# Kernel tuning notes

Hardware: AMD Instinct MI355X
Metric: run time of the kernel (lower is better)

The kernel has to match this reference:

```python
import jax, jax.numpy as jnp
import numpy as np

EMBED = 1024
HEADS = 16
HEAD_DIM = EMBED // HEADS


def setup_inputs() -> dict:
    key = jax.random.key(0)
    k1, k2, k3, k4, k5 = jax.random.split(key, 5)
    x = jax.random.normal(k1, (2, 2048, EMBED), dtype=jnp.float32)
    # torch nn.Linear params: weight [out, in], bias [out]; y = x @ W.T + b
    s_attn = 1.0 / np.sqrt(EMBED)
    w_attn = jax.random.uniform(k2, (3 * EMBED, EMBED), jnp.float32, -s_attn, s_attn)
    b_attn = jax.random.uniform(k3, (3 * EMBED,), jnp.float32, -s_attn, s_attn)
    w_proj = jax.random.uniform(k4, (EMBED, EMBED), jnp.float32, -s_attn, s_attn)
    b_proj = jax.random.uniform(k5, (EMBED,), jnp.float32, -s_attn, s_attn)
    return {"x": x, "w_attn": w_attn, "b_attn": b_attn, "w_proj": w_proj, "b_proj": b_proj}


def reference(x, w_attn, b_attn, w_proj, b_proj):
    B, S, D = x.shape
    qkv = x @ w_attn.T + b_attn                      # [B, S, 3D]
    q, k, v = jnp.split(qkv, 3, axis=-1)             # each [B, S, D]

    def heads(t):  # [B, S, D] -> [B, H, S, hd]
        return t.reshape(B, S, HEADS, HEAD_DIM).transpose(0, 2, 1, 3)

    q, k, v = heads(q), heads(k), heads(v)
    # Faithful to source: NO 1/sqrt(d) scaling, NO causal mask.
    w = jnp.einsum('bhqd,bhkd->bhqk', q, k)          # [B, H, S, S]
    w = jax.nn.softmax(w, axis=-1)
    a = jnp.einsum('bhqk,bhkd->bhqd', w, v)          # [B, H, S, hd]
    a = a.transpose(0, 2, 1, 3).reshape(B, S, D)     # merge heads
    return a @ w_proj.T + b_proj
```

## Files before the change

kernel.cpp:

```cpp
#include <hip/hip_runtime.h>
#include <hip/hip_bf16.h>
#include <stdint.h>
#include <math.h>


typedef __attribute__((ext_vector_type(2))) float f32x2;
typedef __attribute__((ext_vector_type(4))) float f32x4;
typedef __attribute__((ext_vector_type(16))) float f32x16;
typedef __attribute__((ext_vector_type(8))) short bf16x8;

static __device__ __forceinline__ unsigned short f2bf(float f) {
    unsigned u = __float_as_uint(f);
    u += 0x7FFFu + ((u >> 16) & 1u);
    return (unsigned short)(u >> 16);
}
static __device__ __forceinline__ unsigned cvt_pk_bf16(float a, float b) {
    unsigned r;
    asm("v_cvt_pk_bf16_f32 %0, %1, %2" : "=v"(r) : "v"(a), "v"(b));
    return r;
}
static __device__ __forceinline__ float fexp2(float x) {
    float r;
    asm("v_exp_f32 %0, %1" : "=v"(r) : "v"(x));
    return r;
}

typedef const __attribute__((address_space(1))) unsigned int* gas_ptr;
typedef __attribute__((address_space(3))) unsigned int* las_ptr;
static __device__ __forceinline__ void gload_lds16(const void* g, void* l) {
    __builtin_amdgcn_global_load_lds((gas_ptr)g, (las_ptr)l, 16, 0, 0);
}

__global__ void conv_all_kernel(const float* __restrict__ x,
                                const float* __restrict__ wa,
                                unsigned short* __restrict__ x1,
                                unsigned short* __restrict__ w1a) {
    int i = blockIdx.x * blockDim.x + threadIdx.x;
    int stride = gridDim.x * blockDim.x;
    for (; i < 1835008; i += stride) {
        const float* s; unsigned short* d; int j;
        if (i < 1048576)      { s = x;  d = x1;  j = i; }
        else                  { s = wa; d = w1a; j = i - 1048576; }
        float4 v = ((const float4*)s)[j];
        ushort4 o;
        o.x = f2bf(v.x); o.y = f2bf(v.y); o.z = f2bf(v.z); o.w = f2bf(v.w);
        ((ushort4*)d)[j] = o;
    }
}

__global__ __launch_bounds__(256, 2) void gemm_qkv_kernel(
    const unsigned short* __restrict__ A,
    const unsigned short* __restrict__ Bw,
    const float* __restrict__ bias,
    unsigned short* __restrict__ q1,
    unsigned short* __restrict__ k1,
    unsigned short* __restrict__ vT,
    int N, int K)
{
    __shared__ __align__(16) unsigned char lds[34816];
    const int t  = threadIdx.x;
    const int lane = t & 63;
    const int w  = t >> 6;
    const int wr = w >> 1, wc = w & 1;
    const int lg = lane >> 4, ll = lane & 15;

    const int gx = gridDim.x;
    const int flat = blockIdx.y * gx + blockIdx.x;
    const int cpx = (gx * gridDim.y) >> 3;
    const int swz = (flat & 7) * cpx + (flat >> 3);
    const int m0 = (swz / gx) * 128;
    const int n0 = (swz % gx) * 128;

    f32x4 acc[4][4] = {};

    const int srow  = t >> 3;
    const int sslot = t & 7;
    const unsigned short* Abase[4];
    const unsigned short* Bbase[4];
#pragma unroll
    for (int ci = 0; ci < 4; ++ci) {
        int r  = ci * 32 + srow;
        int cg = sslot ^ (r & 7);
        Abase[ci] = A  + (size_t)(m0 + r) * K + cg * 8;
        Bbase[ci] = Bw + (size_t)(n0 + r) * K + cg * 8;
    }

    for (int k0 = 0; k0 < K; k0 += 64) {
#pragma unroll
        for (int ci = 0; ci < 4; ++ci)
            gload_lds16(Abase[ci] + k0, lds + ci*4096 + (t>>6)*1024);
#pragma unroll
        for (int ci = 0; ci < 4; ++ci)
            gload_lds16(Bbase[ci] + k0, lds + 16384 + ci*4096 + (t>>6)*1024);
        __syncthreads();

        bf16x8 af[4][2], bfr[4][2];
#pragma unroll
        for (int mt = 0; mt < 4; ++mt)
#pragma unroll
            for (int kc = 0; kc < 2; ++kc) {
                int row = wr*64 + mt*16 + ll;
                int cg  = (4*kc + lg) ^ (row & 7);
                af[mt][kc] = *(const bf16x8*)(lds + row*128 + cg*16);
            }
#pragma unroll
        for (int nt = 0; nt < 4; ++nt)
#pragma unroll
            for (int kc = 0; kc < 2; ++kc) {
                int row = wc*64 + nt*16 + ll;
                int cg  = (4*kc + lg) ^ (row & 7);
                bfr[nt][kc] = *(const bf16x8*)(lds + 16384 + row*128 + cg*16);
            }
#pragma unroll
        for (int kc = 0; kc < 2; ++kc)
#pragma unroll
            for (int mt = 0; mt < 4; ++mt)
#pragma unroll
                for (int nt = 0; nt < 4; ++nt)
                    acc[mt][nt] = __builtin_amdgcn_mfma_f32_16x16x32_bf16(
                        af[mt][kc], bfr[nt][kc], acc[mt][nt], 0, 0, 0);
        __syncthreads();
    }

    const int TYPE = n0 >> 10;
    unsigned short* l16 = (unsigned short*)lds;
#pragma unroll
    for (int mt = 0; mt < 4; ++mt)
#pragma unroll
      for (int nt = 0; nt < 4; ++nt)
#pragma unroll
        for (int r = 0; r < 4; ++r) {
            int mp = wr*64 + mt*16 + 4*lg + r;
            int np = wc*64 + nt*16 + ll;
            float v = acc[mt][nt][r] + bias[n0 + np];
            if (TYPE == 0) v *= 1.44269504f;
            unsigned short h16 = f2bf(v);
            if (TYPE == 2) l16[np*136 + mp] = h16;
            else           l16[mp*136 + np] = h16;
        }
    __syncthreads();
    {
        const int r2 = t >> 1, half = t & 1;
        const unsigned short* src = l16 + r2*136 + half*64;
        unsigned short* dst;
        if (TYPE == 2) {
            int n = n0 + r2;
            int h = (n >> 6) & 15, d = n & 63;
            int bb = m0 >> 11;
            dst = vT + ((size_t)(bb*16 + h)*64 + d)*2048 + (m0 & 2047) + half*64;
        } else {
            int m = m0 + r2;
            int bb = m >> 11, s = m & 2047;
            int h = ((n0 + half*64) >> 6) & 15;
            dst = (TYPE == 0 ? q1 : k1) + ((size_t)(bb*16 + h)*2048 + s)*64;
        }
#pragma unroll
        for (int j = 0; j < 8; ++j)
            *(uint4*)(dst + j*8) = *(const uint4*)(src + j*8);
    }
}

__global__ __launch_bounds__(256, 2) void gemm_proj_kernel(
    const unsigned short* __restrict__ A,
    const unsigned short* __restrict__ Bw,
    const float* __restrict__ bias,
    float* __restrict__ outp)
{
    __shared__ __align__(16) unsigned char lds[24576];
    const int t  = threadIdx.x;
    const int lane = t & 63;
    const int w  = t >> 6;
    const int lg = lane >> 4, ll = lane & 15;

    const int flat = blockIdx.y * 16 + blockIdx.x;
    const int swz = (flat & 7) * 64 + (flat >> 3);
    const int m0 = (swz >> 4) * 128;
    const int n0 = (swz & 15) * 64;

    f32x4 acc[2][4] = {};

    const int srow  = t >> 3;
    const int sslot = t & 7;
    const unsigned short* Abase[4];
    const unsigned short* Bbase[2];
#pragma unroll
    for (int ci = 0; ci < 4; ++ci) {
        int r  = ci * 32 + srow;
        int cg = sslot ^ (r & 7);
        Abase[ci] = A + (size_t)(m0 + r) * 1024 + cg * 8;
    }
#pragma unroll
    for (int ci = 0; ci < 2; ++ci) {
        int r  = ci * 32 + srow;
        int cg = sslot ^ (r & 7);
        Bbase[ci] = Bw + (size_t)(n0 + r) * 1024 + cg * 8;
    }

    for (int k0 = 0; k0 < 1024; k0 += 64) {
#pragma unroll
        for (int ci = 0; ci < 4; ++ci)
            gload_lds16(Abase[ci] + k0, lds + ci*4096 + w*1024);
#pragma unroll
        for (int ci = 0; ci < 2; ++ci)
            gload_lds16(Bbase[ci] + k0, lds + 16384 + ci*4096 + w*1024);
        __syncthreads();

        bf16x8 af[2][2], bfr[4][2];
#pragma unroll
        for (int mt = 0; mt < 2; ++mt)
#pragma unroll
            for (int kc = 0; kc < 2; ++kc) {
                int row = w*32 + mt*16 + ll;
                int cg  = (4*kc + lg) ^ (row & 7);
                af[mt][kc] = *(const bf16x8*)(lds + row*128 + cg*16);
            }
#pragma unroll
        for (int nt = 0; nt < 4; ++nt)
#pragma unroll
            for (int kc = 0; kc < 2; ++kc) {
                int row = nt*16 + ll;
                int cg  = (4*kc + lg) ^ (row & 7);
                bfr[nt][kc] = *(const bf16x8*)(lds + 16384 + row*128 + cg*16);
            }
#pragma unroll
        for (int kc = 0; kc < 2; ++kc)
#pragma unroll
            for (int mt = 0; mt < 2; ++mt)
#pragma unroll
                for (int nt = 0; nt < 4; ++nt)
                    acc[mt][nt] = __builtin_amdgcn_mfma_f32_16x16x32_bf16(
                        af[mt][kc], bfr[nt][kc], acc[mt][nt], 0, 0, 0);
        __syncthreads();
    }

#pragma unroll
    for (int mt = 0; mt < 2; ++mt)
#pragma unroll
      for (int nt = 0; nt < 4; ++nt)
#pragma unroll
        for (int r = 0; r < 4; ++r) {
            int m = m0 + w*32 + mt*16 + 4*lg + r;
            int n = n0 + nt*16 + ll;
            outp[(size_t)m * 1024 + n] = acc[mt][nt][r] + bias[n];
        }
}

__global__ __launch_bounds__(512, 4) void attn_kernel(
    const unsigned short* __restrict__ q1,
    const unsigned short* __restrict__ k1,
    const unsigned short* __restrict__ vT,
    unsigned short* __restrict__ aout,
    const float* __restrict__ wp,
    unsigned short* __restrict__ wpb)
{
    __shared__ __align__(16) unsigned char lds[65536];
    const int t = threadIdx.x, lane = t & 63, w = t >> 6;
    const int D  = blockIdx.x;

    if (D >= 512) {
        int i = (D - 512) * 512 + t;
        for (; i < 262144; i += 32768) {
            float4 v = ((const float4*)wp)[i];
            ushort4 o;
            o.x = f2bf(v.x); o.y = f2bf(v.y); o.z = f2bf(v.z); o.w = f2bf(v.w);
            ((ushort4*)wpb)[i] = o;
        }
        return;
    }

    const int hi = lane >> 5, lq = lane & 31, l7 = lane & 7;
    const int gp = w >> 2, sw = w & 3;

    const int bh = (D & 7) + ((D >> 7) << 3);
    const int qb = (D >> 3) & 15;
    const int q0 = qb * 128 + sw * 32;

    bf16x8 qf[4];
    {
        const unsigned short* qp = q1 + ((size_t)bh*2048 + q0 + lq)*64 + hi*8;
#pragma unroll
        for (int ks = 0; ks < 4; ++ks)
            qf[ks] = *(const bf16x8*)(qp + ks*16);
    }

    f32x16 o0 = {}, o1 = {};
    f32x2 lr2 = {0.f, 0.f};
    const f32x16 fz = {};

    const int sr = t >> 3, ss = t & 7;
    const int scg = ss ^ (sr & 7);
    const int psr = (sr & 51) | ((sr & 4) << 1) | ((sr & 8) >> 1);
    const unsigned short* Ksrc = k1 + ((size_t)bh*2048 + psr)*64 + scg*8;
    const unsigned short* Vsrc = vT + ((size_t)bh*64 + sr)*2048 + scg*8;
    const int sdst = w*1024;

    unsigned char* fb0 = lds + gp*8192 + lq*128 + (((0 + hi) ^ l7) << 4);
    unsigned char* fb1 = lds + gp*8192 + lq*128 + (((2 + hi) ^ l7) << 4);
    unsigned char* fb2 = lds + gp*8192 + lq*128 + (((4 + hi) ^ l7) << 4);
    unsigned char* fb3 = lds + gp*8192 + lq*128 + (((6 + hi) ^ l7) << 4);

    gload_lds16(Ksrc,        lds + sdst);
    gload_lds16(Ksrc + 4096, lds + 8192 + sdst);
    gload_lds16(Vsrc,        lds + 32768 + sdst);
    gload_lds16(Vsrc + 64,   lds + 32768 + 8192 + sdst);
    __syncthreads();

#define SOFT_PACK(SV, PA, PB)                                                 \
    {                                                                         \
        float e0 =fexp2(SV[0]),  e1 =fexp2(SV[1]),  e2 =fexp2(SV[2]);         \
        float e3 =fexp2(SV[3]),  e4 =fexp2(SV[4]),  e5 =fexp2(SV[5]);         \
        float e6 =fexp2(SV[6]),  e7 =fexp2(SV[7]),  e8 =fexp2(SV[8]);         \
        float e9 =fexp2(SV[9]),  e10=fexp2(SV[10]), e11=fexp2(SV[11]);        \
        float e12=fexp2(SV[12]), e13=fexp2(SV[13]), e14=fexp2(SV[14]);        \
        float e15=fexp2(SV[15]);                                              \
        union { unsigned u[4]; bf16x8 v; } A_, B_;                            \
        A_.u[0]=cvt_pk_bf16(e0,e1);   A_.u[1]=cvt_pk_bf16(e2,e3);             \
        A_.u[2]=cvt_pk_bf16(e4,e5);   A_.u[3]=cvt_pk_bf16(e6,e7);             \
        B_.u[0]=cvt_pk_bf16(e8,e9);   B_.u[1]=cvt_pk_bf16(e10,e11);           \
        B_.u[2]=cvt_pk_bf16(e12,e13); B_.u[3]=cvt_pk_bf16(e14,e15);           \
        PA = A_.v; PB = B_.v;                                                 \
        f32x2 p0 = {e0,e1};   p0 += (f32x2){e2,e3};                           \
        p0 += (f32x2){e4,e5};   p0 += (f32x2){e6,e7};                         \
        p0 += (f32x2){e8,e9};   p0 += (f32x2){e10,e11};                       \
        p0 += (f32x2){e12,e13}; p0 += (f32x2){e14,e15};                       \
        lr2 += p0;                                                            \
    }

#define ATTN_STEP(PAR)                                                        \
    {                                                                         \
        f32x16 s0, s1;                                                        \
        bf16x8 kf;                                                            \
        __builtin_amdgcn_s_setprio(1);                                        \
        kf = *(const bf16x8*)(fb0 + (PAR)*16384);                             \
        s0 = __builtin_amdgcn_mfma_f32_32x32x16_bf16(kf, qf[0], fz, 0,0,0);   \
        kf = *(const bf16x8*)(fb1 + (PAR)*16384);                             \
        s0 = __builtin_amdgcn_mfma_f32_32x32x16_bf16(kf, qf[1], s0, 0,0,0);   \
        kf = *(const bf16x8*)(fb2 + (PAR)*16384);                             \
        s0 = __builtin_amdgcn_mfma_f32_32x32x16_bf16(kf, qf[2], s0, 0,0,0);   \
        kf = *(const bf16x8*)(fb3 + (PAR)*16384);                             \
        s0 = __builtin_amdgcn_mfma_f32_32x32x16_bf16(kf, qf[3], s0, 0,0,0);   \
        kf = *(const bf16x8*)(fb0 + (PAR)*16384 + 4096);                      \
        s1 = __builtin_amdgcn_mfma_f32_32x32x16_bf16(kf, qf[0], fz, 0,0,0);   \
        kf = *(const bf16x8*)(fb1 + (PAR)*16384 + 4096);                      \
        s1 = __builtin_amdgcn_mfma_f32_32x32x16_bf16(kf, qf[1], s1, 0,0,0);   \
        kf = *(const bf16x8*)(fb2 + (PAR)*16384 + 4096);                      \
        s1 = __builtin_amdgcn_mfma_f32_32x32x16_bf16(kf, qf[2], s1, 0,0,0);   \
        kf = *(const bf16x8*)(fb3 + (PAR)*16384 + 4096);                      \
        s1 = __builtin_amdgcn_mfma_f32_32x32x16_bf16(kf, qf[3], s1, 0,0,0);   \
        __builtin_amdgcn_s_setprio(0);                                        \
        bf16x8 pa0, pa1, pa2, pa3;                                            \
        SOFT_PACK(s0, pa0, pa1)                                               \
        bf16x8 vf;                                                            \
        __builtin_amdgcn_s_setprio(1);                                        \
        vf = *(const bf16x8*)(fb0 + (PAR)*16384 + 32768);                     \
        o0 = __builtin_amdgcn_mfma_f32_32x32x16_bf16(pa0, vf, o0, 0,0,0);     \
        vf = *(const bf16x8*)(fb0 + (PAR)*16384 + 32768 + 4096);              \
        o1 = __builtin_amdgcn_mfma_f32_32x32x16_bf16(pa0, vf, o1, 0,0,0);     \
        vf = *(const bf16x8*)(fb1 + (PAR)*16384 + 32768);                     \
        o0 = __builtin_amdgcn_mfma_f32_32x32x16_bf16(pa1, vf, o0, 0,0,0);     \
        vf = *(const bf16x8*)(fb1 + (PAR)*16384 + 32768 + 4096);              \
        o1 = __builtin_amdgcn_mfma_f32_32x32x16_bf16(pa1, vf, o1, 0,0,0);     \
        __builtin_amdgcn_s_setprio(0);                                        \
        SOFT_PACK(s1, pa2, pa3)                                               \
        __builtin_amdgcn_s_setprio(1);                                        \
        vf = *(const bf16x8*)(fb2 + (PAR)*16384 + 32768);                     \
        o0 = __builtin_amdgcn_mfma_f32_32x32x16_bf16(pa2, vf, o0, 0,0,0);     \
        vf = *(const bf16x8*)(fb2 + (PAR)*16384 + 32768 + 4096);              \
        o1 = __builtin_amdgcn_mfma_f32_32x32x16_bf16(pa2, vf, o1, 0,0,0);     \
        vf = *(const bf16x8*)(fb3 + (PAR)*16384 + 32768);                     \
        o0 = __builtin_amdgcn_mfma_f32_32x32x16_bf16(pa3, vf, o0, 0,0,0);     \
        vf = *(const bf16x8*)(fb3 + (PAR)*16384 + 32768 + 4096);              \
        o1 = __builtin_amdgcn_mfma_f32_32x32x16_bf16(pa3, vf, o1, 0,0,0);     \
        __builtin_amdgcn_s_setprio(0);                                        \
    }

    for (int sp = 0; sp < 8; ++sp) {
        {
            const size_t T = 4*(size_t)sp + 2;
            gload_lds16(Ksrc + T*4096,        lds + 16384 + sdst);
            gload_lds16(Ksrc + T*4096 + 4096, lds + 24576 + sdst);
            gload_lds16(Vsrc + T*64,          lds + 32768 + 16384 + sdst);
            gload_lds16(Vsrc + T*64 + 64,     lds + 32768 + 24576 + sdst);
            ATTN_STEP(0)
            __syncthreads();
        }
        {
            if (sp < 7) {
                const size_t T = 4*(size_t)sp + 4;
                gload_lds16(Ksrc + T*4096,        lds + sdst);
                gload_lds16(Ksrc + T*4096 + 4096, lds + 8192 + sdst);
                gload_lds16(Vsrc + T*64,          lds + 32768 + sdst);
                gload_lds16(Vsrc + T*64 + 64,     lds + 32768 + 8192 + sdst);
            }
            ATTN_STEP(1)
            __syncthreads();
        }
    }
#undef ATTN_STEP
#undef SOFT_PACK

    float lrow = lr2[0] + lr2[1];
    lrow += __shfl_xor(lrow, 32);

    float* mb = (float*)lds;
    const int slot = (sw << 6) + lane;
    if (gp == 1) {
        float* p = mb + slot * 36;
#pragma unroll
        for (int c = 0; c < 4; ++c) {
            f32x4 v = { o0[4*c], o0[4*c+1], o0[4*c+2], o0[4*c+3] };
            *(f32x4*)(p + 4*c) = v;
        }
#pragma unroll
        for (int c = 0; c < 4; ++c) {
            f32x4 v = { o1[4*c], o1[4*c+1], o1[4*c+2], o1[4*c+3] };
            *(f32x4*)(p + 16 + 4*c) = v;
        }
        p[32] = lrow;
    }
    __syncthreads();
    if (gp == 0) {
        const float* p = mb + slot * 36;
#pragma unroll
        for (int c = 0; c < 4; ++c) {
            f32x4 v = *(const f32x4*)(p + 4*c);
            o0[4*c] += v[0]; o0[4*c+1] += v[1]; o0[4*c+2] += v[2]; o0[4*c+3] += v[3];
        }
#pragma unroll
        for (int c = 0; c < 4; ++c) {
            f32x4 v = *(const f32x4*)(p + 16 + 4*c);
            o1[4*c] += v[0]; o1[4*c+1] += v[1]; o1[4*c+2] += v[2]; o1[4*c+3] += v[3];
        }
        lrow += p[32];

        const float linv_own = 1.0f / lrow;
        const int bb = bh >> 4, h = bh & 15;
#pragma unroll
        for (int r = 0; r < 16; ++r) {
            int qrow = (r & 3) + 8*(r >> 2) + 4*hi;
            float linv = __shfl(linv_own, qrow);
            size_t srow = q0 + qrow;
            aout[((size_t)(bb*2048 + srow)*16 + h)*64 + lq]      = f2bf(o0[r] * linv);
            aout[((size_t)(bb*2048 + srow)*16 + h)*64 + 32 + lq] = f2bf(o1[r] * linv);
        }
    }
}

extern "C" void kernel_launch(void* const* d_in, const int* in_sizes, int n_in,
                              void* d_out, int out_size, void* d_ws, size_t ws_size,
                              hipStream_t stream) {
    const float* x      = (const float*)d_in[0];
    const float* w_attn = (const float*)d_in[1];
    const float* b_attn = (const float*)d_in[2];
    const float* w_proj = (const float*)d_in[3];
    const float* b_proj = (const float*)d_in[4];
    float* out = (float*)d_out;

    unsigned char* ws = (unsigned char*)d_ws;
    unsigned short* x1  = (unsigned short*)(ws);
    unsigned short* w1a = (unsigned short*)(ws + (size_t)8*1024*1024);
    unsigned short* wpb = (unsigned short*)(ws + (size_t)14*1024*1024);
    unsigned short* q1  = (unsigned short*)(ws + (size_t)16*1024*1024);
    unsigned short* k1  = (unsigned short*)(ws + (size_t)24*1024*1024);
    unsigned short* vT  = (unsigned short*)(ws + (size_t)32*1024*1024);
    unsigned short* ab  = (unsigned short*)(ws + (size_t)40*1024*1024);

    conv_all_kernel<<<1792, 256, 0, stream>>>(x, w_attn, x1, w1a);

    gemm_qkv_kernel<<<dim3(24, 32), 256, 0, stream>>>(
        x1, w1a, b_attn, q1, k1, vT, 3072, 1024);

    attn_kernel<<<576, 512, 0, stream>>>(q1, k1, vT, ab, w_proj, wpb);

    gemm_proj_kernel<<<dim3(16, 32), 256, 0, stream>>>(ab, wpb, b_proj, out);
}
```

Measured before the change: 102.5 us.

## Software-pipeline QK of next tile with softmax/PV of current tile

Restructures the attention main loop so the QK^T MFMAs for tile i are issued after the softmax and PV for tile i-1, giving each step independent MFMA work to overlap the exp/pack latency. V gets a triple-buffered LDS ring (LDS grows from 64KB to 80KB) while K stays double-buffered, and a prologue and epilogue are added. The larger LDS footprint can reduce blocks per CU, and the extra live s0/s1 registers raise register pressure.

Result: no change. 103.2 us (+0.7%).

```diff
diff --git a/kernel.cpp b/kernel.cpp
--- a/kernel.cpp
+++ b/kernel.cpp
@@ -253,7 +253,7 @@
     const float* __restrict__ wp,
     unsigned short* __restrict__ wpb)
 {
-    __shared__ __align__(16) unsigned char lds[65536];
+    __shared__ __align__(16) unsigned char lds[81920];
     const int t = threadIdx.x, lane = t & 63, w = t >> 6;
     const int D  = blockIdx.x;
 
@@ -298,12 +298,11 @@
     unsigned char* fb1 = lds + gp*8192 + lq*128 + (((2 + hi) ^ l7) << 4);
     unsigned char* fb2 = lds + gp*8192 + lq*128 + (((4 + hi) ^ l7) << 4);
     unsigned char* fb3 = lds + gp*8192 + lq*128 + (((6 + hi) ^ l7) << 4);
-
-    gload_lds16(Ksrc,        lds + sdst);
-    gload_lds16(Ksrc + 4096, lds + 8192 + sdst);
-    gload_lds16(Vsrc,        lds + 32768 + sdst);
-    gload_lds16(Vsrc + 64,   lds + 32768 + 8192 + sdst);
-    __syncthreads();
+    unsigned char* vbase = lds + 32768 + gp*8192 + lq*128;
+    const int vx0 = (((0 + hi) ^ l7) << 4);
+    const int vx1 = (((2 + hi) ^ l7) << 4);
+    const int vx2 = (((4 + hi) ^ l7) << 4);
+    const int vx3 = (((6 + hi) ^ l7) << 4);
 
 #define SOFT_PACK(SV, PA, PB)                                                 \
     {                                                                         \
@@ -326,77 +325,92 @@
         lr2 += p0;                                                            \
     }
 
-#define ATTN_STEP(PAR)                                                        \
+#define QK_CORE(KP)                                                           \
     {                                                                         \
-        f32x16 s0, s1;                                                        \
         bf16x8 kf;                                                            \
         __builtin_amdgcn_s_setprio(1);                                        \
-        kf = *(const bf16x8*)(fb0 + (PAR)*16384);                             \
+        kf = *(const bf16x8*)(fb0 + (KP));                                    \
         s0 = __builtin_amdgcn_mfma_f32_32x32x16_bf16(kf, qf[0], fz, 0,0,0);   \
-        kf = *(const bf16x8*)(fb1 + (PAR)*16384);                             \
+        kf = *(const bf16x8*)(fb1 + (KP));                                    \
         s0 = __builtin_amdgcn_mfma_f32_32x32x16_bf16(kf, qf[1], s0, 0,0,0);   \
-        kf = *(const bf16x8*)(fb2 + (PAR)*16384);                             \
+        kf = *(const bf16x8*)(fb2 + (KP));                                    \
         s0 = __builtin_amdgcn_mfma_f32_32x32x16_bf16(kf, qf[2], s0, 0,0,0);   \
-        kf = *(const bf16x8*)(fb3 + (PAR)*16384);                             \
+        kf = *(const bf16x8*)(fb3 + (KP));                                    \
         s0 = __builtin_amdgcn_mfma_f32_32x32x16_bf16(kf, qf[3], s0, 0,0,0);   \
-        kf = *(const bf16x8*)(fb0 + (PAR)*16384 + 4096);                      \
+        kf = *(const bf16x8*)(fb0 + (KP) + 4096);                             \
         s1 = __builtin_amdgcn_mfma_f32_32x32x16_bf16(kf, qf[0], fz, 0,0,0);   \
-        kf = *(const bf16x8*)(fb1 + (PAR)*16384 + 4096);                      \
+        kf = *(const bf16x8*)(fb1 + (KP) + 4096);                             \
         s1 = __builtin_amdgcn_mfma_f32_32x32x16_bf16(kf, qf[1], s1, 0,0,0);   \
-        kf = *(const bf16x8*)(fb2 + (PAR)*16384 + 4096);                      \
+        kf = *(const bf16x8*)(fb2 + (KP) + 4096);                             \
         s1 = __builtin_amdgcn_mfma_f32_32x32x16_bf16(kf, qf[2], s1, 0,0,0);   \
-        kf = *(const bf16x8*)(fb3 + (PAR)*16384 + 4096);                      \
+        kf = *(const bf16x8*)(fb3 + (KP) + 4096);                             \
         s1 = __builtin_amdgcn_mfma_f32_32x32x16_bf16(kf, qf[3], s1, 0,0,0);   \
         __builtin_amdgcn_s_setprio(0);                                        \
-        bf16x8 pa0, pa1, pa2, pa3;                                            \
-        SOFT_PACK(s0, pa0, pa1)                                               \
+    }
+
+#define PV_HALF(VP, PA, PB, X0, X1)                                           \
+    {                                                                         \
         bf16x8 vf;                                                            \
         __builtin_amdgcn_s_setprio(1);                                        \
-        vf = *(const bf16x8*)(fb0 + (PAR)*16384 + 32768);                     \
-        o0 = __builtin_amdgcn_mfma_f32_32x32x16_bf16(pa0, vf, o0, 0,0,0);     \
-        vf = *(const bf16x8*)(fb0 + (PAR)*16384 + 32768 + 4096);              \
-        o1 = __builtin_amdgcn_mfma_f32_32x32x16_bf16(pa0, vf, o1, 0,0,0);     \
-        vf = *(const bf16x8*)(fb1 + (PAR)*16384 + 32768);                     \
-        o0 = __builtin_amdgcn_mfma_f32_32x32x16_bf16(pa1, vf, o0, 0,0,0);     \
-        vf = *(const bf16x8*)(fb1 + (PAR)*16384 + 32768 + 4096);              \
-        o1 = __builtin_amdgcn_mfma_f32_32x32x16_bf16(pa1, vf, o1, 0,0,0);     \
+        vf = *(const bf16x8*)((VP) + (X0));                                   \
+        o0 = __builtin_amdgcn_mfma_f32_32x32x16_bf16(PA, vf, o0, 0,0,0);      \
+        vf = *(const bf16x8*)((VP) + (X0) + 4096);                            \
+        o1 = __builtin_amdgcn_mfma_f32_32x32x16_bf16(PA, vf, o1, 0,0,0);      \
+        vf = *(const bf16x8*)((VP) + (X1));                                   \
+        o0 = __builtin_amdgcn_mfma_f32_32x32x16_bf16(PB, vf, o0, 0,0,0);      \
+        vf = *(const bf16x8*)((VP) + (X1) + 4096);                            \
+        o1 = __builtin_amdgcn_mfma_f32_32x32x16_bf16(PB, vf, o1, 0,0,0);      \
         __builtin_amdgcn_s_setprio(0);                                        \
-        SOFT_PACK(s1, pa2, pa3)                                               \
-        __builtin_amdgcn_s_setprio(1);                                        \
-        vf = *(const bf16x8*)(fb2 + (PAR)*16384 + 32768);                     \
-        o0 = __builtin_amdgcn_mfma_f32_32x32x16_bf16(pa2, vf, o0, 0,0,0);     \
-        vf = *(const bf16x8*)(fb2 + (PAR)*16384 + 32768 + 4096);              \
-        o1 = __builtin_amdgcn_mfma_f32_32x32x16_bf16(pa2, vf, o1, 0,0,0);     \
-        vf = *(const bf16x8*)(fb3 + (PAR)*16384 + 32768);                     \
-        o0 = __builtin_amdgcn_mfma_f32_32x32x16_bf16(pa3, vf, o0, 0,0,0);     \
-        vf = *(const bf16x8*)(fb3 + (PAR)*16384 + 32768 + 4096);              \
-        o1 = __builtin_amdgcn_mfma_f32_32x32x16_bf16(pa3, vf, o1, 0,0,0);     \
-        __builtin_amdgcn_s_setprio(0);                                        \
-    }
-
-    for (int sp = 0; sp < 8; ++sp) {
-        {
-            const size_t T = 4*(size_t)sp + 2;
-            gload_lds16(Ksrc + T*4096,        lds + 16384 + sdst);
-            gload_lds16(Ksrc + T*4096 + 4096, lds + 24576 + sdst);
-            gload_lds16(Vsrc + T*64,          lds + 32768 + 16384 + sdst);
-            gload_lds16(Vsrc + T*64 + 64,     lds + 32768 + 24576 + sdst);
-            ATTN_STEP(0)
-            __syncthreads();
-        }
-        {
-            if (sp < 7) {
-                const size_t T = 4*(size_t)sp + 4;
-                gload_lds16(Ksrc + T*4096,        lds + sdst);
-                gload_lds16(Ksrc + T*4096 + 4096, lds + 8192 + sdst);
-                gload_lds16(Vsrc + T*64,          lds + 32768 + sdst);
-                gload_lds16(Vsrc + T*64 + 64,     lds + 32768 + 8192 + sdst);
-            }
-            ATTN_STEP(1)
-            __syncthreads();
-        }
-    }
-#undef ATTN_STEP
+    }
+
+    f32x16 s0, s1;
+
+    gload_lds16(Ksrc,        lds + sdst);
+    gload_lds16(Ksrc + 4096, lds + 8192 + sdst);
+    gload_lds16(Vsrc,        lds + 32768 + sdst);
+    gload_lds16(Vsrc + 64,   lds + 32768 + 8192 + sdst);
+    __syncthreads();
+    gload_lds16(Ksrc + (size_t)2*4096, lds + 16384 + sdst);
+    gload_lds16(Ksrc + (size_t)3*4096, lds + 16384 + 8192 + sdst);
+    gload_lds16(Vsrc + 2*64,           lds + 32768 + 16384 + sdst);
+    gload_lds16(Vsrc + 3*64,           lds + 32768 + 16384 + 8192 + sdst);
+    QK_CORE(0)
+    __syncthreads();
+
+    int vrd = 0;
+    int vst = 32768;
+    for (int i = 1; i < 16; ++i) {
+        const int kcur  = (i & 1) << 14;
+        if (i < 15) {
+            const int knext = ((i + 1) & 1) << 14;
+            const size_t T2 = 2*(size_t)(i + 1);
+            gload_lds16(Ksrc + T2*4096,     lds + knext + sdst);
+            gload_lds16(Ksrc + (T2+1)*4096, lds + knext + 8192 + sdst);
+            gload_lds16(Vsrc + T2*64,       lds + 32768 + vst + sdst);
+            gload_lds16(Vsrc + (T2+1)*64,   lds + 32768 + vst + 8192 + sdst);
+        }
+        bf16x8 pa0, pa1, pa2, pa3;
+        unsigned char* vp = vbase + vrd;
+        SOFT_PACK(s0, pa0, pa1)
+        PV_HALF(vp, pa0, pa1, vx0, vx1)
+        SOFT_PACK(s1, pa2, pa3)
+        PV_HALF(vp, pa2, pa3, vx2, vx3)
+        QK_CORE(kcur)
+        __syncthreads();
+        vrd = (vrd == 32768) ? 0 : vrd + 16384;
+        vst = (vst == 32768) ? 0 : vst + 16384;
+    }
+    {
+        bf16x8 pa0, pa1, pa2, pa3;
+        unsigned char* vp = vbase + vrd;
+        SOFT_PACK(s0, pa0, pa1)
+        PV_HALF(vp, pa0, pa1, vx0, vx1)
+        SOFT_PACK(s1, pa2, pa3)
+        PV_HALF(vp, pa2, pa3, vx2, vx3)
+    }
+    __syncthreads();
+#undef PV_HALF
+#undef QK_CORE
 #undef SOFT_PACK
 
     float lrow = lr2[0] + lr2[1];
```
